# Kernel tuning notes

Measured on AMD Instinct MI355X. Metric: run time of the kernel, lower is better.

The kernel has to match this reference:

```python
import jax, jax.numpy as jnp
import numpy as np

D_MODEL = 1024
N_HEADS = 16
D_K = D_MODEL // N_HEADS
D_FF = 4096
B = 2
T = 2048


def _layernorm(x, gamma, beta, eps=1e-5):
    mu = jnp.mean(x, axis=-1, keepdims=True)
    var = jnp.var(x, axis=-1, keepdims=True)
    return (x - mu) * jax.lax.rsqrt(var + eps) * gamma + beta


def _attention(q_in, kv_in, Wq, bq, Wk, bk, Wv, bv, mask):
    # q_in: [B,Tq,D], kv_in: [B,Tk,D]; Wq/Wk/Wv: [H,D,d_k]; b*: [H,d_k]
    Q = jnp.einsum('btd,hdk->bhtk', q_in, Wq) + bq[None, :, None, :]
    K = jnp.einsum('bsd,hdk->bhsk', kv_in, Wk) + bk[None, :, None, :]
    V = jnp.einsum('bsd,hdk->bhsk', kv_in, Wv) + bv[None, :, None, :]
    scores = jnp.einsum('bhtk,bhsk->bhts', Q, K) / jnp.sqrt(jnp.asarray(D_K, Q.dtype))
    if mask is not None:
        scores = jnp.where(mask, scores, jnp.finfo(scores.dtype).min)
    attn = jax.nn.softmax(scores, axis=-1)
    out = jnp.einsum('bhts,bhsk->bhtk', attn, V)  # [B,H,Tq,d_k]
    # concat heads: [B,Tq,H*d_k] == [B,Tq,D]
    return out.transpose(0, 2, 1, 3).reshape(q_in.shape[0], q_in.shape[1], -1)


def setup_inputs() -> dict:
    key = jax.random.key(0)
    ks = jax.random.split(key, 24)
    s = 0.02
    inp = {
        'dec_input': jax.random.normal(ks[0], (B, T, D_MODEL), jnp.float32),
        'enc_output': jax.random.normal(ks[1], (B, T, D_MODEL), jnp.float32),
        # self-attention per-head weights stacked over heads
        'Wq_s': jax.random.normal(ks[2], (N_HEADS, D_MODEL, D_K), jnp.float32) * s,
        'bq_s': jnp.zeros((N_HEADS, D_K), jnp.float32),
        'Wk_s': jax.random.normal(ks[3], (N_HEADS, D_MODEL, D_K), jnp.float32) * s,
        'bk_s': jnp.zeros((N_HEADS, D_K), jnp.float32),
        'Wv_s': jax.random.normal(ks[4], (N_HEADS, D_MODEL, D_K), jnp.float32) * s,
        'bv_s': jnp.zeros((N_HEADS, D_K), jnp.float32),
        'Wo_s': jax.random.normal(ks[5], (D_MODEL, D_MODEL), jnp.float32) * s,
        'bo_s': jnp.zeros((D_MODEL,), jnp.float32),
        # cross-attention per-head weights
        'Wq_c': jax.random.normal(ks[6], (N_HEADS, D_MODEL, D_K), jnp.float32) * s,
        'bq_c': jnp.zeros((N_HEADS, D_K), jnp.float32),
        'Wk_c': jax.random.normal(ks[7], (N_HEADS, D_MODEL, D_K), jnp.float32) * s,
        'bk_c': jnp.zeros((N_HEADS, D_K), jnp.float32),
        'Wv_c': jax.random.normal(ks[8], (N_HEADS, D_MODEL, D_K), jnp.float32) * s,
        'bv_c': jnp.zeros((N_HEADS, D_K), jnp.float32),
        'Wo_c': jax.random.normal(ks[9], (D_MODEL, D_MODEL), jnp.float32) * s,
        'bo_c': jnp.zeros((D_MODEL,), jnp.float32),
        # FFN
        'W1': jax.random.normal(ks[10], (D_MODEL, D_FF), jnp.float32) * s,
        'b1': jnp.zeros((D_FF,), jnp.float32),
        'W2': jax.random.normal(ks[11], (D_FF, D_MODEL), jnp.float32) * s,
        'b2': jnp.zeros((D_MODEL,), jnp.float32),
        # layernorms
        'g1': jnp.ones((D_MODEL,), jnp.float32), 'be1': jnp.zeros((D_MODEL,), jnp.float32),
        'g2': jnp.ones((D_MODEL,), jnp.float32), 'be2': jnp.zeros((D_MODEL,), jnp.float32),
        'g3': jnp.ones((D_MODEL,), jnp.float32), 'be3': jnp.zeros((D_MODEL,), jnp.float32),
    }
    return inp


def reference(dec_input, enc_output,
              Wq_s, bq_s, Wk_s, bk_s, Wv_s, bv_s, Wo_s, bo_s,
              Wq_c, bq_c, Wk_c, bk_c, Wv_c, bv_c, Wo_c, bo_c,
              W1, b1, W2, b2, g1, be1, g2, be2, g3, be3):
    Tq = dec_input.shape[1]
    causal = jnp.tril(jnp.ones((Tq, Tq), bool))[None, None, :, :]  # [1,1,T,T]
    # masked multi-head self-attention (dropout is identity in eval)
    sa = _attention(dec_input, dec_input, Wq_s, bq_s, Wk_s, bk_s, Wv_s, bv_s, causal)
    sa = sa @ Wo_s.T if False else jnp.einsum('btd,ed->bte', sa, Wo_s.T) if False else sa @ Wo_s + bo_s
    x1 = _layernorm(dec_input + sa, g1, be1)
    # cross-attention (no mask)
    ca = _attention(x1, enc_output, Wq_c, bq_c, Wk_c, bk_c, Wv_c, bv_c, None)
    ca = ca @ Wo_c + bo_c
    x2 = _layernorm(x1 + ca, g2, be2)
    # FFN
    ffn = jax.nn.relu(x2 @ W1 + b1) @ W2 + b2
    x3 = _layernorm(x2 + ffn, g3, be3)
    return x3
```

## Files before the change

kernel.cpp:

```cpp
#include <hip/hip_runtime.h>
#include <hip/hip_bf16.h>

typedef __attribute__((ext_vector_type(8))) short short8;
typedef __attribute__((ext_vector_type(4))) float floatx4;

#define TDIM 2048
#define BDIM 2
#define MROWS (BDIM * TDIM)

#define ASM_VMCNT0() __asm__ volatile("s_waitcnt vmcnt(0)" ::: "memory")
#define ASM_LGKM0()  __asm__ volatile("s_waitcnt lgkmcnt(0)" ::: "memory")
#define ASM_BARRIER() __asm__ volatile("s_barrier" ::: "memory")

__device__ __forceinline__ void gload_lds16(const void* g, void* l) {
    __builtin_amdgcn_global_load_lds((const __attribute__((address_space(1))) void*)g,
                                     (__attribute__((address_space(3))) void*)l, 16, 0, 0);
}

__global__ __launch_bounds__(256) void cast_bf16_k(const float* __restrict__ in,
                                                   __hip_bfloat16* __restrict__ out) {
    size_t i = ((size_t)blockIdx.x * 256 + threadIdx.x) * 4;
    float4 v = *(const float4*)&in[i];
    out[i + 0] = __float2bfloat16(v.x);
    out[i + 1] = __float2bfloat16(v.y);
    out[i + 2] = __float2bfloat16(v.z);
    out[i + 3] = __float2bfloat16(v.w);
}

__global__ __launch_bounds__(256) void transpose_cast_k(const float* __restrict__ in,
                                                        __hip_bfloat16* __restrict__ out,
                                                        int R, int C) {
    __shared__ float tile[32][33];
    const size_t slab = (size_t)blockIdx.z * R * C;
    in += slab;
    out += slab;
    const int c0 = blockIdx.x * 32, r0 = blockIdx.y * 32;
    const int tx = threadIdx.x & 31, ty = threadIdx.x >> 5;
#pragma unroll
    for (int i = 0; i < 4; ++i)
        tile[ty + 8 * i][tx] = in[(size_t)(r0 + ty + 8 * i) * C + c0 + tx];
    __syncthreads();
#pragma unroll
    for (int i = 0; i < 4; ++i)
        out[(size_t)(c0 + ty + 8 * i) * R + r0 + tx] = __float2bfloat16(tile[tx][ty + 8 * i]);
}

__global__ void concat3_k(const float* __restrict__ a, const float* __restrict__ b,
                          const float* __restrict__ c, float* __restrict__ o) {
    int i = blockIdx.x * 256 + threadIdx.x;
    o[i] = (i < 1024) ? a[i] : (i < 2048 ? b[i - 1024] : c[i - 2048]);
}
__global__ void concat2_k(const float* __restrict__ a, const float* __restrict__ b,
                          float* __restrict__ o) {
    int i = blockIdx.x * 256 + threadIdx.x;
    o[i] = (i < 1024) ? a[i] : b[i - 1024];
}

__device__ __forceinline__ void gemm_core(
    const __hip_bfloat16* __restrict__ A, const __hip_bfloat16* __restrict__ Bt,
    int K, int kBeg, int kLen,
    const float* __restrict__ bias, __hip_bfloat16* __restrict__ C, int ldc,
    float* __restrict__ Pf,
    __hip_bfloat16* __restrict__ Vt, int vt_col0, int relu,
    int m0, int n0, __hip_bfloat16* sm) {
    const int tid = threadIdx.x;
    const int lane = tid & 63, wave = tid >> 6;
    const int quad = lane >> 4, l16 = lane & 15;
    const int wm = (wave >> 1) * 64, wn = (wave & 1) * 64;
    const int lrow = lane >> 3;
    const int gsw = (((lane & 7) ^ lrow)) * 8;
    const int sw7 = l16 & 7;
    const __hip_bfloat16* gA = A + (size_t)(m0 + wave * 32 + lrow) * K + kBeg + gsw;
    const __hip_bfloat16* gB = Bt + (size_t)(n0 + wave * 32 + lrow) * K + kBeg + gsw;
    __hip_bfloat16* lA = sm + wave * 2048;
    __hip_bfloat16* lB = sm + 16384 + wave * 2048;
    floatx4 acc[4][4] = {};
    const int T = kLen >> 6;
#pragma unroll
    for (int i = 0; i < 4; ++i) {
        gload_lds16(gA + (size_t)i * 8 * K, lA + i * 512);
        gload_lds16(gB + (size_t)i * 8 * K, lB + i * 512);
    }
    for (int t = 0; t < T; ++t) {
        ASM_VMCNT0();
        ASM_BARRIER();
        if (t + 1 < T) {
            const int koff = (t + 1) << 6;
            const int b = ((t + 1) & 1) * 8192;
#pragma unroll
            for (int i = 0; i < 4; ++i) {
                gload_lds16(gA + (size_t)i * 8 * K + koff, lA + b + i * 512);
                gload_lds16(gB + (size_t)i * 8 * K + koff, lB + b + i * 512);
            }
        }
        const __hip_bfloat16* cA = sm + (t & 1) * 8192;
        const __hip_bfloat16* cB = sm + 16384 + (t & 1) * 8192;
#pragma unroll
        for (int kc = 0; kc < 2; ++kc) {
            short8 af[4], bfr[4];
#pragma unroll
            for (int i = 0; i < 4; ++i) {
                af[i] = *(const short8*)&cA[(wm + i * 16 + l16) * 64 +
                                            (((kc * 4 + quad) ^ sw7) * 8)];
                bfr[i] = *(const short8*)&cB[(wn + i * 16 + l16) * 64 +
                                             (((kc * 4 + quad) ^ sw7) * 8)];
            }
#pragma unroll
            for (int mi = 0; mi < 4; ++mi)
#pragma unroll
                for (int ni = 0; ni < 4; ++ni)
                    acc[mi][ni] =
                        __builtin_amdgcn_mfma_f32_16x16x32_bf16(af[mi], bfr[ni], acc[mi][ni], 0, 0, 0);
        }
    }
    if (Pf) {
#pragma unroll
        for (int ni = 0; ni < 4; ++ni) {
            const int col = n0 + wn + ni * 16 + l16;
#pragma unroll
            for (int mi = 0; mi < 4; ++mi)
#pragma unroll
                for (int r = 0; r < 4; ++r) {
                    const int row = m0 + wm + mi * 16 + quad * 4 + r;
                    Pf[(size_t)row * ldc + col] = acc[mi][ni][r];
                }
        }
    } else {
        const bool toVt = (n0 >= vt_col0);
#pragma unroll
        for (int ni = 0; ni < 4; ++ni) {
            const int col = n0 + wn + ni * 16 + l16;
            const float bv = bias[col];
#pragma unroll
            for (int mi = 0; mi < 4; ++mi)
#pragma unroll
                for (int r = 0; r < 4; ++r) {
                    const int row = m0 + wm + mi * 16 + quad * 4 + r;
                    float v = acc[mi][ni][r] + bv;
                    if (relu) v = fmaxf(v, 0.f);
                    __hip_bfloat16 h = __float2bfloat16(v);
                    if (toVt) {
                        const int b = row >> 11, t = row & (TDIM - 1);
                        Vt[((size_t)(b * 1024 + (col - vt_col0)) << 11) + t] = h;
                    } else {
                        C[(size_t)row * ldc + col] = h;
                    }
                }
        }
    }
}

__global__ __launch_bounds__(256) void gemm_bf16_k(const __hip_bfloat16* __restrict__ A,
                                                   const __hip_bfloat16* __restrict__ Bt,
                                                   const float* __restrict__ bias,
                                                   __hip_bfloat16* __restrict__ C,
                                                   int N, int K, int relu,
                                                   __hip_bfloat16* __restrict__ Vt, int vt_col0) {
    __shared__ __hip_bfloat16 sm[2 * 128 * 64 * 2];
    gemm_core(A, Bt, K, 0, K, bias, C, N, nullptr, Vt, vt_col0, relu,
              blockIdx.y * 128, blockIdx.x * 128, sm);
}

__global__ __launch_bounds__(256) void gemm_sk2_k(const __hip_bfloat16* __restrict__ A,
                                                  const __hip_bfloat16* __restrict__ Bt,
                                                  float* __restrict__ Pf, int N, int K) {
    __shared__ __hip_bfloat16 sm[2 * 128 * 64 * 2];
    const int z = blockIdx.z;
    gemm_core(A, Bt, K, z * (K >> 1), K >> 1, nullptr, nullptr, N,
              Pf + (size_t)z * MROWS * N, nullptr, 1 << 30, 0,
              blockIdx.y * 128, blockIdx.x * 128, sm);
}

__global__ __launch_bounds__(256) void gemm_pair_k(
    const __hip_bfloat16* __restrict__ A1, const __hip_bfloat16* __restrict__ Bt1,
    const float* __restrict__ bias1, __hip_bfloat16* __restrict__ C1, int N1, int K1,
    const __hip_bfloat16* __restrict__ A2, const __hip_bfloat16* __restrict__ Bt2,
    const float* __restrict__ bias2, __hip_bfloat16* __restrict__ C2, int N2, int K2,
    __hip_bfloat16* __restrict__ Vt2, int vtc2, int nx1) {
    __shared__ __hip_bfloat16 sm[2 * 128 * 64 * 2];
    if ((int)blockIdx.x < nx1)
        gemm_core(A1, Bt1, K1, 0, K1, bias1, C1, N1, nullptr, nullptr, 1 << 30, 0,
                  blockIdx.y * 128, blockIdx.x * 128, sm);
    else
        gemm_core(A2, Bt2, K2, 0, K2, bias2, C2, N2, nullptr, Vt2, vtc2, 0,
                  blockIdx.y * 128, (blockIdx.x - nx1) * 128, sm);
}

__device__ __forceinline__ void flash_one(
    const __hip_bfloat16* __restrict__ Q, int ldq, int qc0,
    const __hip_bfloat16* __restrict__ Kp, int ldk,
    const __hip_bfloat16* __restrict__ Vp,
    __hip_bfloat16* __restrict__ O, int causal, int q0, size_t rowb, int h,
    __hip_bfloat16* sK, __hip_bfloat16* sV, __hip_bfloat16* sP) {
    const int tid = threadIdx.x, lane = tid & 63, wave = tid >> 6;
    const int quad = lane >> 4, l16 = lane & 15;
    const int lrow = lane >> 3;
    const int gsw = ((lane & 7) ^ lrow) * 8;
    const int sw7 = l16 & 7;
    short8 qf[2];
    {
        const __hip_bfloat16* qp = Q + (rowb + q0 + wave * 16 + l16) * (size_t)ldq + qc0 + h * 64;
        const float qs = 0.18033688f;
        short8 r0 = *(const short8*)(qp + quad * 8);
        short8 r1 = *(const short8*)(qp + 32 + quad * 8);
#pragma unroll
        for (int j = 0; j < 8; ++j) {
            float f0 = __uint_as_float(((unsigned)(unsigned short)r0[j]) << 16) * qs;
            float f1 = __uint_as_float(((unsigned)(unsigned short)r1[j]) << 16) * qs;
            __hip_bfloat16 h0 = __float2bfloat16(f0), h1 = __float2bfloat16(f1);
            qf[0][j] = *(short*)&h0;
            qf[1][j] = *(short*)&h1;
        }
    }
    short8 ones;
#pragma unroll
    for (int j = 0; j < 8; ++j) ones[j] = (short)0x3F80;
    floatx4 Of[4] = {};
    floatx4 accl = {};
    const int nDiag = q0 >> 6;
    const int lastT = causal ? nDiag : (TDIM >> 6) - 1;
    ASM_LGKM0();
    ASM_BARRIER();
#pragma unroll
    for (int i = 0; i < 2; ++i) {
        const int rb = wave * 16 + i * 8;
        gload_lds16(&Kp[(rowb + rb + lrow) * (size_t)ldk + gsw], &sK[rb * 64]);
        gload_lds16(&Vp[(size_t)(rb + lrow) * TDIM + gsw], &sV[rb * 64]);
    }
    for (int t = 0; t <= lastT; ++t) {
        ASM_VMCNT0();
        ASM_BARRIER();
        if (t < lastT) {
            const int s1 = (t + 1) << 6, nb = ((t + 1) & 1) * 4096;
#pragma unroll
            for (int i = 0; i < 2; ++i) {
                const int rb = wave * 16 + i * 8;
                gload_lds16(&Kp[(rowb + s1 + rb + lrow) * (size_t)ldk + gsw], &sK[nb + rb * 64]);
                gload_lds16(&Vp[(size_t)(rb + lrow) * TDIM + s1 + gsw], &sV[nb + rb * 64]);
            }
        }
        const int cb = (t & 1) * 4096;
        floatx4 Sf[4] = {};
#pragma unroll
        for (int nt = 0; nt < 4; ++nt) {
            short8 b0 = *(const short8*)&sK[cb + (nt * 16 + l16) * 64 + ((quad ^ sw7) * 8)];
            short8 b1 = *(const short8*)&sK[cb + (nt * 16 + l16) * 64 + (((4 + quad) ^ sw7) * 8)];
            Sf[nt] = __builtin_amdgcn_mfma_f32_16x16x32_bf16(qf[0], b0, Sf[nt], 0, 0, 0);
            Sf[nt] = __builtin_amdgcn_mfma_f32_16x16x32_bf16(qf[1], b1, Sf[nt], 0, 0, 0);
        }
#pragma unroll
        for (int nt = 0; nt < 4; ++nt)
#pragma unroll
            for (int r = 0; r < 4; ++r) Sf[nt][r] = exp2f(Sf[nt][r]);
        if (causal && t == nDiag) {
#pragma unroll
            for (int nt = 0; nt < 4; ++nt) {
                const int sc = nt * 16 + l16;
#pragma unroll
                for (int r = 0; r < 4; ++r) {
                    const int qr = wave * 16 + quad * 4 + r;
                    if (sc > qr) Sf[nt][r] = 0.f;
                }
            }
        }
#pragma unroll
        for (int nt = 0; nt < 4; ++nt)
#pragma unroll
            for (int r = 0; r < 4; ++r) {
                const int row = quad * 4 + r;
                sP[wave * 1024 + row * 64 + (((nt * 2 + (l16 >> 3)) ^ (row & 7)) * 8) + (l16 & 7)] =
                    __float2bfloat16(Sf[nt][r]);
            }
        ASM_LGKM0();
        short8 pf0 = *(const short8*)&sP[wave * 1024 + l16 * 64 + ((quad ^ sw7) * 8)];
        short8 pf1 = *(const short8*)&sP[wave * 1024 + l16 * 64 + (((4 + quad) ^ sw7) * 8)];
        accl = __builtin_amdgcn_mfma_f32_16x16x32_bf16(pf0, ones, accl, 0, 0, 0);
        accl = __builtin_amdgcn_mfma_f32_16x16x32_bf16(pf1, ones, accl, 0, 0, 0);
#pragma unroll
        for (int d = 0; d < 4; ++d) {
            short8 v0 = *(const short8*)&sV[cb + (d * 16 + l16) * 64 + ((quad ^ sw7) * 8)];
            short8 v1 = *(const short8*)&sV[cb + (d * 16 + l16) * 64 + (((4 + quad) ^ sw7) * 8)];
            Of[d] = __builtin_amdgcn_mfma_f32_16x16x32_bf16(pf0, v0, Of[d], 0, 0, 0);
            Of[d] = __builtin_amdgcn_mfma_f32_16x16x32_bf16(pf1, v1, Of[d], 0, 0, 0);
        }
    }
#pragma unroll
    for (int r = 0; r < 4; ++r) {
        const float inv = 1.0f / accl[r];
#pragma unroll
        for (int d = 0; d < 4; ++d) {
            O[(rowb + q0 + wave * 16 + quad * 4 + r) * (size_t)1024 + h * 64 + d * 16 + l16] =
                __float2bfloat16(Of[d][r] * inv);
        }
    }
}

__global__ __launch_bounds__(256) void flash_attn(const __hip_bfloat16* __restrict__ Q, int ldq, int qc0,
                                                  const __hip_bfloat16* __restrict__ K, int ldk, int kc0,
                                                  const __hip_bfloat16* __restrict__ Vt,
                                                  __hip_bfloat16* __restrict__ O, int causal) {
    __shared__ __hip_bfloat16 sK[2 * 64 * 64];
    __shared__ __hip_bfloat16 sV[2 * 64 * 64];
    __shared__ __hip_bfloat16 sP[4 * 16 * 64];
    const int bh = blockIdx.y, b = bh >> 4, h = bh & 15;
    const size_t rowb = (size_t)b * TDIM;
    const __hip_bfloat16* Kp = K + kc0 + h * 64;
    const __hip_bfloat16* Vp = Vt + ((size_t)(b * 1024 + h * 64) << 11);
    if (causal) {
        flash_one(Q, ldq, qc0, Kp, ldk, Vp, O, 1, (int)blockIdx.x * 64, rowb, h, sK, sV, sP);
        flash_one(Q, ldq, qc0, Kp, ldk, Vp, O, 1, (31 - (int)blockIdx.x) * 64, rowb, h, sK, sV, sP);
    } else {
        flash_one(Q, ldq, qc0, Kp, ldk, Vp, O, 0, (int)blockIdx.x * 64, rowb, h, sK, sV, sP);
    }
}

__global__ __launch_bounds__(256) void ln2_k(const float* __restrict__ resid,
                                             const float* __restrict__ d0,
                                             const float* __restrict__ d1,
                                             const float* __restrict__ biasN,
                                             const float* __restrict__ gamma,
                                             const float* __restrict__ beta,
                                             float* __restrict__ outf,
                                             __hip_bfloat16* __restrict__ outb) {
    const int row = blockIdx.x, tid = threadIdx.x;
    const size_t base = (size_t)row * 1024;
    float x[4], s = 0.f, sq = 0.f;
#pragma unroll
    for (int i = 0; i < 4; ++i) {
        const int c = tid + 256 * i;
        x[i] = resid[base + c] + d0[base + c] + d1[base + c] + biasN[c];
        s += x[i];
        sq += x[i] * x[i];
    }
#pragma unroll
    for (int off = 32; off > 0; off >>= 1) {
        s += __shfl_down(s, off);
        sq += __shfl_down(sq, off);
    }
    __shared__ float red[8];
    if ((tid & 63) == 0) {
        red[tid >> 6] = s;
        red[4 + (tid >> 6)] = sq;
    }
    __syncthreads();
    const float S = red[0] + red[1] + red[2] + red[3];
    const float Q2 = red[4] + red[5] + red[6] + red[7];
    const float mean = S * (1.f / 1024.f);
    const float var = Q2 * (1.f / 1024.f) - mean * mean;
    const float rstd = rsqrtf(var + 1e-5f);
#pragma unroll
    for (int i = 0; i < 4; ++i) {
        const int c = tid + 256 * i;
        const float y = (x[i] - mean) * rstd * gamma[c] + beta[c];
        outf[base + c] = y;
        outb[base + c] = __float2bfloat16(y);
    }
}

extern "C" void kernel_launch(void* const* d_in, const int* in_sizes, int n_in,
                              void* d_out, int out_size, void* d_ws, size_t ws_size,
                              hipStream_t stream) {
    (void)in_sizes; (void)n_in; (void)out_size; (void)ws_size;
    const float* dec  = (const float*)d_in[0];
    const float* enc  = (const float*)d_in[1];
    const float* Wq_s = (const float*)d_in[2];
    const float* bq_s = (const float*)d_in[3];
    const float* Wk_s = (const float*)d_in[4];
    const float* bk_s = (const float*)d_in[5];
    const float* Wv_s = (const float*)d_in[6];
    const float* bv_s = (const float*)d_in[7];
    const float* Wo_s = (const float*)d_in[8];
    const float* bo_s = (const float*)d_in[9];
    const float* Wq_c = (const float*)d_in[10];
    const float* bq_c = (const float*)d_in[11];
    const float* Wk_c = (const float*)d_in[12];
    const float* bk_c = (const float*)d_in[13];
    const float* Wv_c = (const float*)d_in[14];
    const float* bv_c = (const float*)d_in[15];
    const float* Wo_c = (const float*)d_in[16];
    const float* bo_c = (const float*)d_in[17];
    const float* W1   = (const float*)d_in[18];
    const float* b1   = (const float*)d_in[19];
    const float* W2   = (const float*)d_in[20];
    const float* b2   = (const float*)d_in[21];
    const float* g1   = (const float*)d_in[22];
    const float* be1  = (const float*)d_in[23];
    const float* g2   = (const float*)d_in[24];
    const float* be2  = (const float*)d_in[25];
    const float* g3   = (const float*)d_in[26];
    const float* be3  = (const float*)d_in[27];

    char* w = (char*)d_ws;
    const size_t MB = 1ull << 20;
    __hip_bfloat16* Xdec   = (__hip_bfloat16*)(w + 0 * MB);
    __hip_bfloat16* Xenc   = (__hip_bfloat16*)(w + 8 * MB);
    __hip_bfloat16* WtQKVs = (__hip_bfloat16*)(w + 16 * MB);
    __hip_bfloat16* WtOs   = (__hip_bfloat16*)(w + 22 * MB);
    __hip_bfloat16* WtQc   = (__hip_bfloat16*)(w + 24 * MB);
    __hip_bfloat16* WtKVc  = (__hip_bfloat16*)(w + 26 * MB);
    __hip_bfloat16* WtOc   = (__hip_bfloat16*)(w + 30 * MB);
    __hip_bfloat16* Wt1    = (__hip_bfloat16*)(w + 32 * MB);
    __hip_bfloat16* Wt2    = (__hip_bfloat16*)(w + 40 * MB);
    float*          BiasQKVs = (float*)(w + 48 * MB);
    float*          BiasKVc  = (float*)(w + 48 * MB + 65536);
    __hip_bfloat16* QKV    = (__hip_bfloat16*)(w + 49 * MB);
    __hip_bfloat16* Qc     = QKV;
    __hip_bfloat16* KVc    = (__hip_bfloat16*)(w + 57 * MB);
    float*          Psplit = (float*)(w + 49 * MB);
    __hip_bfloat16* VtBuf  = (__hip_bfloat16*)(w + 73 * MB);
    __hip_bfloat16* Attn   = (__hip_bfloat16*)(w + 81 * MB);
    float*          X1f    = (float*)(w + 97 * MB);
    __hip_bfloat16* X1b    = (__hip_bfloat16*)(w + 113 * MB);
    float*          X2f    = (float*)(w + 121 * MB);
    __hip_bfloat16* X2b    = (__hip_bfloat16*)(w + 137 * MB);
    __hip_bfloat16* H1     = (__hip_bfloat16*)(w + 145 * MB);
    float*          P0     = Psplit;
    float*          P1     = Psplit + (size_t)MROWS * 1024;
    const int NOVT = 1 << 30;

    cast_bf16_k<<<4096, 256, 0, stream>>>(dec, Xdec);
    cast_bf16_k<<<4096, 256, 0, stream>>>(enc, Xenc);
    transpose_cast_k<<<dim3(2, 32, 16), 256, 0, stream>>>(Wq_s, WtQKVs + 0ull * 1024 * 1024, 1024, 64);
    transpose_cast_k<<<dim3(2, 32, 16), 256, 0, stream>>>(Wk_s, WtQKVs + 1ull * 1024 * 1024, 1024, 64);
    transpose_cast_k<<<dim3(2, 32, 16), 256, 0, stream>>>(Wv_s, WtQKVs + 2ull * 1024 * 1024, 1024, 64);
    transpose_cast_k<<<dim3(2, 32, 16), 256, 0, stream>>>(Wq_c, WtQc, 1024, 64);
    transpose_cast_k<<<dim3(2, 32, 16), 256, 0, stream>>>(Wk_c, WtKVc + 0ull * 1024 * 1024, 1024, 64);
    transpose_cast_k<<<dim3(2, 32, 16), 256, 0, stream>>>(Wv_c, WtKVc + 1ull * 1024 * 1024, 1024, 64);
    transpose_cast_k<<<dim3(32, 32, 1), 256, 0, stream>>>(Wo_s, WtOs, 1024, 1024);
    transpose_cast_k<<<dim3(32, 32, 1), 256, 0, stream>>>(Wo_c, WtOc, 1024, 1024);
    transpose_cast_k<<<dim3(128, 32, 1), 256, 0, stream>>>(W1, Wt1, 1024, 4096);
    transpose_cast_k<<<dim3(32, 128, 1), 256, 0, stream>>>(W2, Wt2, 4096, 1024);
    concat3_k<<<12, 256, 0, stream>>>(bq_s, bk_s, bv_s, BiasQKVs);
    concat2_k<<<8, 256, 0, stream>>>(bk_c, bv_c, BiasKVc);

    gemm_bf16_k<<<dim3(24, 32), 256, 0, stream>>>(Xdec, WtQKVs, BiasQKVs, QKV, 3072, 1024, 0,
                                                  VtBuf, 2048);
    flash_attn<<<dim3(16, 32), 256, 0, stream>>>(QKV, 3072, 0, QKV, 3072, 1024, VtBuf, Attn, 1);
    gemm_sk2_k<<<dim3(8, 32, 2), 256, 0, stream>>>(Attn, WtOs, Psplit, 1024, 1024);
    ln2_k<<<MROWS, 256, 0, stream>>>(dec, P0, P1, bo_s, g1, be1, X1f, X1b);

    gemm_pair_k<<<dim3(24, 32), 256, 0, stream>>>(X1b, WtQc, bq_c, Qc, 1024, 1024,
                                                  Xenc, WtKVc, BiasKVc, KVc, 2048, 1024,
                                                  VtBuf, 1024, 8);
    flash_attn<<<dim3(32, 32), 256, 0, stream>>>(Qc, 1024, 0, KVc, 2048, 0, VtBuf, Attn, 0);
    gemm_sk2_k<<<dim3(8, 32, 2), 256, 0, stream>>>(Attn, WtOc, Psplit, 1024, 1024);
    ln2_k<<<MROWS, 256, 0, stream>>>(X1f, P0, P1, bo_c, g2, be2, X2f, X2b);

    gemm_bf16_k<<<dim3(32, 32), 256, 0, stream>>>(X2b, Wt1, b1, H1, 4096, 1024, 1,
                                                  (__hip_bfloat16*)nullptr, NOVT);
    gemm_sk2_k<<<dim3(8, 32, 2), 256, 0, stream>>>(H1, Wt2, Psplit, 1024, 4096);
    ln2_k<<<MROWS, 256, 0, stream>>>(X2f, P0, P1, b2, g3, be3, (float*)d_out, X1b);
}
```

Baseline: 598.6 us.

## Keep attention probabilities in registers, batch prep kernels, vectorize Vt stores

The flash-attention inner loop now computes S transposed (K as the A operand), so the exponentiated scores already sit in the B-operand layout of a 16x16x16 MFMA. P no longer round-trips through shared memory and the LDS wait is gone. The row-sum and PV products use the smaller MFMA, and output stores are packed four at a time. Separately, the 14 weight/bias/input prep launches are merged into two kernels, and the V-transpose epilogue writes 4-element vectors. The trade-off is twice as many, smaller MFMAs for PV and a compile-time fallback if the 1k builtin is missing.

After: 546.9 us. 1.09x faster.

```diff
diff --git a/kernel.cpp b/kernel.cpp
--- a/kernel.cpp
+++ b/kernel.cpp
@@ -2,6 +2,7 @@
 #include <hip/hip_bf16.h>
 
 typedef __attribute__((ext_vector_type(8))) short short8;
+typedef __attribute__((ext_vector_type(4))) short short4v;
 typedef __attribute__((ext_vector_type(4))) float floatx4;
 
 #define TDIM 2048
@@ -12,29 +13,49 @@
 #define ASM_LGKM0()  __asm__ volatile("s_waitcnt lgkmcnt(0)" ::: "memory")
 #define ASM_BARRIER() __asm__ volatile("s_barrier" ::: "memory")
 
+__device__ __forceinline__ floatx4 mfma16(short4v a, short4v b, floatx4 c) {
+#if defined(__HIP_DEVICE_COMPILE__)
+#if __has_builtin(__builtin_amdgcn_mfma_f32_16x16x16bf16_1k)
+    return __builtin_amdgcn_mfma_f32_16x16x16bf16_1k(a, b, c, 0, 0, 0);
+#else
+    short8 az = {a[0], a[1], a[2], a[3], 0, 0, 0, 0};
+    short8 bz = {b[0], b[1], b[2], b[3], 0, 0, 0, 0};
+    return __builtin_amdgcn_mfma_f32_16x16x32_bf16(az, bz, c, 0, 0, 0);
+#endif
+#else
+    (void)a; (void)b;
+    return c;
+#endif
+}
+
 __device__ __forceinline__ void gload_lds16(const void* g, void* l) {
     __builtin_amdgcn_global_load_lds((const __attribute__((address_space(1))) void*)g,
                                      (__attribute__((address_space(3))) void*)l, 16, 0, 0);
 }
 
-__global__ __launch_bounds__(256) void cast_bf16_k(const float* __restrict__ in,
-                                                   __hip_bfloat16* __restrict__ out) {
-    size_t i = ((size_t)blockIdx.x * 256 + threadIdx.x) * 4;
-    float4 v = *(const float4*)&in[i];
-    out[i + 0] = __float2bfloat16(v.x);
-    out[i + 1] = __float2bfloat16(v.y);
-    out[i + 2] = __float2bfloat16(v.z);
-    out[i + 3] = __float2bfloat16(v.w);
-}
-
-__global__ __launch_bounds__(256) void transpose_cast_k(const float* __restrict__ in,
-                                                        __hip_bfloat16* __restrict__ out,
-                                                        int R, int C) {
-    __shared__ float tile[32][33];
-    const size_t slab = (size_t)blockIdx.z * R * C;
-    in += slab;
-    out += slab;
-    const int c0 = blockIdx.x * 32, r0 = blockIdx.y * 32;
+__device__ __forceinline__ short bf16s(float x) {
+    __hip_bfloat16 h = __float2bfloat16(x);
+    return *(short*)&h;
+}
+
+__global__ __launch_bounds__(256) void cast2_k(const float* __restrict__ a,
+                                               const float* __restrict__ b,
+                                               __hip_bfloat16* __restrict__ oa,
+                                               __hip_bfloat16* __restrict__ ob) {
+    const int blk = blockIdx.x;
+    const float* in = (blk < 4096) ? a : b;
+    __hip_bfloat16* out = (blk < 4096) ? oa : ob;
+    const size_t base = (size_t)(blk & 4095) * 1024 + threadIdx.x * 4;
+    float4 v = *(const float4*)&in[base];
+    out[base + 0] = __float2bfloat16(v.x);
+    out[base + 1] = __float2bfloat16(v.y);
+    out[base + 2] = __float2bfloat16(v.z);
+    out[base + 3] = __float2bfloat16(v.w);
+}
+
+__device__ __forceinline__ void t32(float (*tile)[33], const float* __restrict__ in,
+                                    __hip_bfloat16* __restrict__ out, int R, int C,
+                                    int c0, int r0) {
     const int tx = threadIdx.x & 31, ty = threadIdx.x >> 5;
 #pragma unroll
     for (int i = 0; i < 4; ++i)
@@ -45,15 +66,51 @@
         out[(size_t)(c0 + ty + 8 * i) * R + r0 + tx] = __float2bfloat16(tile[tx][ty + 8 * i]);
 }
 
-__global__ void concat3_k(const float* __restrict__ a, const float* __restrict__ b,
-                          const float* __restrict__ c, float* __restrict__ o) {
-    int i = blockIdx.x * 256 + threadIdx.x;
-    o[i] = (i < 1024) ? a[i] : (i < 2048 ? b[i - 1024] : c[i - 2048]);
-}
-__global__ void concat2_k(const float* __restrict__ a, const float* __restrict__ b,
-                          float* __restrict__ o) {
-    int i = blockIdx.x * 256 + threadIdx.x;
-    o[i] = (i < 1024) ? a[i] : b[i - 1024];
+__global__ __launch_bounds__(256) void prep_w_k(
+    const float* __restrict__ Wq_s, const float* __restrict__ Wk_s, const float* __restrict__ Wv_s,
+    const float* __restrict__ Wq_c, const float* __restrict__ Wk_c, const float* __restrict__ Wv_c,
+    const float* __restrict__ Wo_s, const float* __restrict__ Wo_c,
+    const float* __restrict__ W1, const float* __restrict__ W2,
+    const float* __restrict__ bq_s, const float* __restrict__ bk_s, const float* __restrict__ bv_s,
+    const float* __restrict__ bk_c, const float* __restrict__ bv_c,
+    __hip_bfloat16* __restrict__ WtQKVs, __hip_bfloat16* __restrict__ WtQc,
+    __hip_bfloat16* __restrict__ WtKVc, __hip_bfloat16* __restrict__ WtOs,
+    __hip_bfloat16* __restrict__ WtOc, __hip_bfloat16* __restrict__ Wt1,
+    __hip_bfloat16* __restrict__ Wt2,
+    float* __restrict__ BiasQKVs, float* __restrict__ BiasKVc) {
+    __shared__ float tile[32][33];
+    const int t = blockIdx.x;
+    if (t < 6144) {
+        const int seg = t >> 10, tl = t & 1023;
+        const float* s;
+        __hip_bfloat16* d;
+        if (seg == 0) { s = Wq_s; d = WtQKVs; }
+        else if (seg == 1) { s = Wk_s; d = WtQKVs + 1048576; }
+        else if (seg == 2) { s = Wv_s; d = WtQKVs + 2097152; }
+        else if (seg == 3) { s = Wq_c; d = WtQc; }
+        else if (seg == 4) { s = Wk_c; d = WtKVc; }
+        else { s = Wv_c; d = WtKVc + 1048576; }
+        const int slab = tl >> 6, rem = tl & 63;
+        t32(tile, s + (size_t)slab * 65536, d + (size_t)slab * 65536, 1024, 64,
+            (rem & 1) * 32, (rem >> 1) * 32);
+    } else if (t < 8192) {
+        const int rem = (t - 6144) & 1023;
+        const float* s = (t < 7168) ? Wo_s : Wo_c;
+        __hip_bfloat16* d = (t < 7168) ? WtOs : WtOc;
+        t32(tile, s, d, 1024, 1024, (rem & 31) * 32, (rem >> 5) * 32);
+    } else if (t < 12288) {
+        const int rem = t - 8192;
+        t32(tile, W1, Wt1, 1024, 4096, (rem & 127) * 32, (rem >> 7) * 32);
+    } else if (t < 16384) {
+        const int rem = t - 12288;
+        t32(tile, W2, Wt2, 4096, 1024, (rem & 31) * 32, (rem >> 5) * 32);
+    } else if (t < 16396) {
+        const int i = (t - 16384) * 256 + threadIdx.x;
+        BiasQKVs[i] = (i < 1024) ? bq_s[i] : (i < 2048 ? bk_s[i - 1024] : bv_s[i - 2048]);
+    } else {
+        const int i = (t - 16396) * 256 + threadIdx.x;
+        BiasKVc[i] = (i < 1024) ? bk_c[i] : bv_c[i - 1024];
+    }
 }
 
 __device__ __forceinline__ void gemm_core(
@@ -132,20 +189,23 @@
             const int col = n0 + wn + ni * 16 + l16;
             const float bv = bias[col];
 #pragma unroll
-            for (int mi = 0; mi < 4; ++mi)
-#pragma unroll
-                for (int r = 0; r < 4; ++r) {
-                    const int row = m0 + wm + mi * 16 + quad * 4 + r;
-                    float v = acc[mi][ni][r] + bv;
-                    if (relu) v = fmaxf(v, 0.f);
-                    __hip_bfloat16 h = __float2bfloat16(v);
-                    if (toVt) {
-                        const int b = row >> 11, t = row & (TDIM - 1);
-                        Vt[((size_t)(b * 1024 + (col - vt_col0)) << 11) + t] = h;
-                    } else {
-                        C[(size_t)row * ldc + col] = h;
+            for (int mi = 0; mi < 4; ++mi) {
+                const int row0 = m0 + wm + mi * 16 + quad * 4;
+                if (toVt) {
+                    const int b = row0 >> 11, t0 = row0 & (TDIM - 1);
+                    short4v pk;
+#pragma unroll
+                    for (int r = 0; r < 4; ++r) pk[r] = bf16s(acc[mi][ni][r] + bv);
+                    *(short4v*)&Vt[((size_t)(b * 1024 + (col - vt_col0)) << 11) + t0] = pk;
+                } else {
+#pragma unroll
+                    for (int r = 0; r < 4; ++r) {
+                        float v = acc[mi][ni][r] + bv;
+                        if (relu) v = fmaxf(v, 0.f);
+                        C[(size_t)(row0 + r) * ldc + col] = __float2bfloat16(v);
                     }
                 }
+            }
         }
     }
 }
@@ -191,7 +251,7 @@
     const __hip_bfloat16* __restrict__ Kp, int ldk,
     const __hip_bfloat16* __restrict__ Vp,
     __hip_bfloat16* __restrict__ O, int causal, int q0, size_t rowb, int h,
-    __hip_bfloat16* sK, __hip_bfloat16* sV, __hip_bfloat16* sP) {
+    __hip_bfloat16* sK, __hip_bfloat16* sV) {
     const int tid = threadIdx.x, lane = tid & 63, wave = tid >> 6;
     const int quad = lane >> 4, l16 = lane & 15;
     const int lrow = lane >> 3;
@@ -205,17 +265,14 @@
         short8 r1 = *(const short8*)(qp + 32 + quad * 8);
 #pragma unroll
         for (int j = 0; j < 8; ++j) {
-            float f0 = __uint_as_float(((unsigned)(unsigned short)r0[j]) << 16) * qs;
-            float f1 = __uint_as_float(((unsigned)(unsigned short)r1[j]) << 16) * qs;
-            __hip_bfloat16 h0 = __float2bfloat16(f0), h1 = __float2bfloat16(f1);
-            qf[0][j] = *(short*)&h0;
-            qf[1][j] = *(short*)&h1;
-        }
-    }
-    short8 ones;
-#pragma unroll
-    for (int j = 0; j < 8; ++j) ones[j] = (short)0x3F80;
-    floatx4 Of[4] = {};
+            qf[0][j] = bf16s(__uint_as_float(((unsigned)(unsigned short)r0[j]) << 16) * qs);
+            qf[1][j] = bf16s(__uint_as_float(((unsigned)(unsigned short)r1[j]) << 16) * qs);
+        }
+    }
+    short4v ones4;
+#pragma unroll
+    for (int j = 0; j < 4; ++j) ones4[j] = (short)0x3F80;
+    floatx4 Ot[4] = {};
     floatx4 accl = {};
     const int nDiag = q0 >> 6;
     const int lastT = causal ? nDiag : (TDIM >> 6) - 1;
@@ -242,56 +299,49 @@
         const int cb = (t & 1) * 4096;
         floatx4 Sf[4] = {};
 #pragma unroll
-        for (int nt = 0; nt < 4; ++nt) {
-            short8 b0 = *(const short8*)&sK[cb + (nt * 16 + l16) * 64 + ((quad ^ sw7) * 8)];
-            short8 b1 = *(const short8*)&sK[cb + (nt * 16 + l16) * 64 + (((4 + quad) ^ sw7) * 8)];
-            Sf[nt] = __builtin_amdgcn_mfma_f32_16x16x32_bf16(qf[0], b0, Sf[nt], 0, 0, 0);
-            Sf[nt] = __builtin_amdgcn_mfma_f32_16x16x32_bf16(qf[1], b1, Sf[nt], 0, 0, 0);
-        }
-#pragma unroll
-        for (int nt = 0; nt < 4; ++nt)
-#pragma unroll
-            for (int r = 0; r < 4; ++r) Sf[nt][r] = exp2f(Sf[nt][r]);
+        for (int st = 0; st < 4; ++st) {
+            short8 b0 = *(const short8*)&sK[cb + (st * 16 + l16) * 64 + ((quad ^ sw7) * 8)];
+            short8 b1 = *(const short8*)&sK[cb + (st * 16 + l16) * 64 + (((4 + quad) ^ sw7) * 8)];
+            Sf[st] = __builtin_amdgcn_mfma_f32_16x16x32_bf16(b0, qf[0], Sf[st], 0, 0, 0);
+            Sf[st] = __builtin_amdgcn_mfma_f32_16x16x32_bf16(b1, qf[1], Sf[st], 0, 0, 0);
+        }
+#pragma unroll
+        for (int st = 0; st < 4; ++st)
+#pragma unroll
+            for (int r = 0; r < 4; ++r) Sf[st][r] = exp2f(Sf[st][r]);
         if (causal && t == nDiag) {
-#pragma unroll
-            for (int nt = 0; nt < 4; ++nt) {
-                const int sc = nt * 16 + l16;
-#pragma unroll
-                for (int r = 0; r < 4; ++r) {
-                    const int qr = wave * 16 + quad * 4 + r;
-                    if (sc > qr) Sf[nt][r] = 0.f;
-                }
+            const int qr = wave * 16 + l16;
+#pragma unroll
+            for (int st = 0; st < 4; ++st)
+#pragma unroll
+                for (int r = 0; r < 4; ++r)
+                    if (st * 16 + quad * 4 + r > qr) Sf[st][r] = 0.f;
+        }
+        short4v pf[4];
+#pragma unroll
+        for (int st = 0; st < 4; ++st)
+#pragma unroll
+            for (int r = 0; r < 4; ++r) pf[st][r] = bf16s(Sf[st][r]);
+#pragma unroll
+        for (int st = 0; st < 4; ++st) accl = mfma16(ones4, pf[st], accl);
+#pragma unroll
+        for (int dt = 0; dt < 4; ++dt)
+#pragma unroll
+            for (int st = 0; st < 4; ++st) {
+                short4v av = *(const short4v*)&sV[cb + (dt * 16 + l16) * 64 +
+                                                 (((st * 2 + (quad >> 1)) ^ sw7) * 8) +
+                                                 (quad & 1) * 4];
+                Ot[dt] = mfma16(av, pf[st], Ot[dt]);
             }
-        }
-#pragma unroll
-        for (int nt = 0; nt < 4; ++nt)
-#pragma unroll
-            for (int r = 0; r < 4; ++r) {
-                const int row = quad * 4 + r;
-                sP[wave * 1024 + row * 64 + (((nt * 2 + (l16 >> 3)) ^ (row & 7)) * 8) + (l16 & 7)] =
-                    __float2bfloat16(Sf[nt][r]);
-            }
-        ASM_LGKM0();
-        short8 pf0 = *(const short8*)&sP[wave * 1024 + l16 * 64 + ((quad ^ sw7) * 8)];
-        short8 pf1 = *(const short8*)&sP[wave * 1024 + l16 * 64 + (((4 + quad) ^ sw7) * 8)];
-        accl = __builtin_amdgcn_mfma_f32_16x16x32_bf16(pf0, ones, accl, 0, 0, 0);
-        accl = __builtin_amdgcn_mfma_f32_16x16x32_bf16(pf1, ones, accl, 0, 0, 0);
-#pragma unroll
-        for (int d = 0; d < 4; ++d) {
-            short8 v0 = *(const short8*)&sV[cb + (d * 16 + l16) * 64 + ((quad ^ sw7) * 8)];
-            short8 v1 = *(const short8*)&sV[cb + (d * 16 + l16) * 64 + (((4 + quad) ^ sw7) * 8)];
-            Of[d] = __builtin_amdgcn_mfma_f32_16x16x32_bf16(pf0, v0, Of[d], 0, 0, 0);
-            Of[d] = __builtin_amdgcn_mfma_f32_16x16x32_bf16(pf1, v1, Of[d], 0, 0, 0);
-        }
-    }
-#pragma unroll
-    for (int r = 0; r < 4; ++r) {
-        const float inv = 1.0f / accl[r];
-#pragma unroll
-        for (int d = 0; d < 4; ++d) {
-            O[(rowb + q0 + wave * 16 + quad * 4 + r) * (size_t)1024 + h * 64 + d * 16 + l16] =
-                __float2bfloat16(Of[d][r] * inv);
-        }
+    }
+    const float inv = 1.0f / accl[0];
+    __hip_bfloat16* op = O + (rowb + q0 + wave * 16 + l16) * (size_t)1024 + h * 64 + quad * 4;
+#pragma unroll
+    for (int dt = 0; dt < 4; ++dt) {
+        short4v pk;
+#pragma unroll
+        for (int r = 0; r < 4; ++r) pk[r] = bf16s(Ot[dt][r] * inv);
+        *(short4v*)(op + dt * 16) = pk;
     }
 }
 
@@ -301,16 +351,15 @@
                                                   __hip_bfloat16* __restrict__ O, int causal) {
     __shared__ __hip_bfloat16 sK[2 * 64 * 64];
     __shared__ __hip_bfloat16 sV[2 * 64 * 64];
-    __shared__ __hip_bfloat16 sP[4 * 16 * 64];
     const int bh = blockIdx.y, b = bh >> 4, h = bh & 15;
     const size_t rowb = (size_t)b * TDIM;
     const __hip_bfloat16* Kp = K + kc0 + h * 64;
     const __hip_bfloat16* Vp = Vt + ((size_t)(b * 1024 + h * 64) << 11);
     if (causal) {
-        flash_one(Q, ldq, qc0, Kp, ldk, Vp, O, 1, (int)blockIdx.x * 64, rowb, h, sK, sV, sP);
-        flash_one(Q, ldq, qc0, Kp, ldk, Vp, O, 1, (31 - (int)blockIdx.x) * 64, rowb, h, sK, sV, sP);
+        flash_one(Q, ldq, qc0, Kp, ldk, Vp, O, 1, (int)blockIdx.x * 64, rowb, h, sK, sV);
+        flash_one(Q, ldq, qc0, Kp, ldk, Vp, O, 1, (31 - (int)blockIdx.x) * 64, rowb, h, sK, sV);
     } else {
-        flash_one(Q, ldq, qc0, Kp, ldk, Vp, O, 0, (int)blockIdx.x * 64, rowb, h, sK, sV, sP);
+        flash_one(Q, ldq, qc0, Kp, ldk, Vp, O, 0, (int)blockIdx.x * 64, rowb, h, sK, sV);
     }
 }
 
@@ -418,20 +467,11 @@
     float*          P1     = Psplit + (size_t)MROWS * 1024;
     const int NOVT = 1 << 30;
 
-    cast_bf16_k<<<4096, 256, 0, stream>>>(dec, Xdec);
-    cast_bf16_k<<<4096, 256, 0, stream>>>(enc, Xenc);
-    transpose_cast_k<<<dim3(2, 32, 16), 256, 0, stream>>>(Wq_s, WtQKVs + 0ull * 1024 * 1024, 1024, 64);
-    transpose_cast_k<<<dim3(2, 32, 16), 256, 0, stream>>>(Wk_s, WtQKVs + 1ull * 1024 * 1024, 1024, 64);
-    transpose_cast_k<<<dim3(2, 32, 16), 256, 0, stream>>>(Wv_s, WtQKVs + 2ull * 1024 * 1024, 1024, 64);
-    transpose_cast_k<<<dim3(2, 32, 16), 256, 0, stream>>>(Wq_c, WtQc, 1024, 64);
-    transpose_cast_k<<<dim3(2, 32, 16), 256, 0, stream>>>(Wk_c, WtKVc + 0ull * 1024 * 1024, 1024, 64);
-    transpose_cast_k<<<dim3(2, 32, 16), 256, 0, stream>>>(Wv_c, WtKVc + 1ull * 1024 * 1024, 1024, 64);
-    transpose_cast_k<<<dim3(32, 32, 1), 256, 0, stream>>>(Wo_s, WtOs, 1024, 1024);
-    transpose_cast_k<<<dim3(32, 32, 1), 256, 0, stream>>>(Wo_c, WtOc, 1024, 1024);
-    transpose_cast_k<<<dim3(128, 32, 1), 256, 0, stream>>>(W1, Wt1, 1024, 4096);
-    transpose_cast_k<<<dim3(32, 128, 1), 256, 0, stream>>>(W2, Wt2, 4096, 1024);
-    concat3_k<<<12, 256, 0, stream>>>(bq_s, bk_s, bv_s, BiasQKVs);
-    concat2_k<<<8, 256, 0, stream>>>(bk_c, bv_c, BiasKVc);
+    cast2_k<<<8192, 256, 0, stream>>>(dec, enc, Xdec, Xenc);
+    prep_w_k<<<16404, 256, 0, stream>>>(Wq_s, Wk_s, Wv_s, Wq_c, Wk_c, Wv_c, Wo_s, Wo_c,
+                                        W1, W2, bq_s, bk_s, bv_s, bk_c, bv_c,
+                                        WtQKVs, WtQc, WtKVc, WtOs, WtOc, Wt1, Wt2,
+                                        BiasQKVs, BiasKVc);
 
     gemm_bf16_k<<<dim3(24, 32), 256, 0, stream>>>(Xdec, WtQKVs, BiasQKVs, QKV, 3072, 1024, 0,
                                                   VtBuf, 2048);
```
